# Kernel tuning notes

Measured on AMD Instinct MI355X. Metric: run time of the kernel, lower is better.

The kernel has to match this reference:

```python
import jax, jax.numpy as jnp
import numpy as np

N_HEAD = 16
N_EMBD = 2048
HEAD_DIM = N_EMBD // N_HEAD


def setup_inputs() -> dict:
    key = jax.random.key(0)
    kx, kqkv, kp = jax.random.split(key, 3)
    B, S = 2, 2048
    x = jax.random.normal(kx, (B, S, N_EMBD), dtype=jnp.float32)
    # torch nn.Linear weights, stored as [out, in]; y = x @ W.T
    scale = 1.0 / np.sqrt(N_EMBD)
    Wqkv = jax.random.uniform(kqkv, (3 * N_EMBD, N_EMBD), dtype=jnp.float32, minval=-scale, maxval=scale)
    Wproj = jax.random.uniform(kp, (N_EMBD, N_EMBD), dtype=jnp.float32, minval=-scale, maxval=scale)
    return {"x": x, "Wqkv": Wqkv, "Wproj": Wproj}


def reference(x, Wqkv, Wproj):
    B, S, E = x.shape
    qkv = x @ Wqkv.T  # [B,S,3E]
    q, k, v = jnp.split(qkv, 3, axis=2)
    # [B,H,S,D]
    q = q.reshape(B, S, N_HEAD, HEAD_DIM).transpose(0, 2, 1, 3)
    k = k.reshape(B, S, N_HEAD, HEAD_DIM).transpose(0, 2, 1, 3)
    v = v.reshape(B, S, N_HEAD, HEAD_DIM).transpose(0, 2, 1, 3)
    scores = jnp.einsum('bhqd,bhkd->bhqk', q, k) / jnp.sqrt(jnp.float32(HEAD_DIM))
    causal = jnp.tril(jnp.ones((S, S), dtype=bool))  # [S,S]
    scores = jnp.where(causal[None, None, :, :], scores, -jnp.inf)
    weights = jax.nn.softmax(scores, axis=-1)
    out = jnp.einsum('bhqk,bhkd->bhqd', weights, v)  # [B,H,S,D]
    out = out.transpose(0, 2, 1, 3).reshape(B, S, E)
    return out @ Wproj.T
```

## Files before the change

kernel.cpp:

```cpp
#include <hip/hip_runtime.h>
#include <cstdint>
#include <cstddef>

typedef __bf16 bf16;
typedef __bf16 bf16x8 __attribute__((ext_vector_type(8)));
typedef float  f32x4  __attribute__((ext_vector_type(4)));

static_assert(sizeof(bf16x8) == 16, "bf16x8 must be 16B");

__device__ __forceinline__ void async_copy16(const bf16* g, bf16* l) {
  __builtin_amdgcn_global_load_lds(
      (__attribute__((address_space(1))) void*)(g),
      (__attribute__((address_space(3))) void*)(l),
      16, 0, 0);
}

__global__ __launch_bounds__(256)
void conv_f32_bf16(const float* __restrict__ s, bf16* __restrict__ d) {
  const size_t i = ((size_t)blockIdx.x * 256 + threadIdx.x) * 8;
  const f32x4 a = *(const f32x4*)(s + i);
  const f32x4 b = *(const f32x4*)(s + i + 4);
  bf16x8 o;
#pragma unroll
  for (int e = 0; e < 4; ++e) { o[e] = (bf16)a[e]; o[4 + e] = (bf16)b[e]; }
  *(bf16x8*)(d + i) = o;
}

template<int AMODE>
__device__ __forceinline__ void stage_half(const bf16* __restrict__ P, int K,
                                           int row0, int k0, int ks,
                                           bf16* lds, int wave, int lane) {
#pragma unroll
  for (int i = 0; i < 2; ++i) {
    const int lin0 = i * 512 + wave * 64;
    const int lin  = lin0 + lane;
    const int row  = lin >> 2;
    const int ch   = lin & 3;
    const int gch  = ch ^ ((row >> 1) & 3);
    const bf16* src;
    if constexpr (AMODE == 2) {
      const int rowA = row0 + row;
      const int b = rowA >> 11, s = rowA & 2047;
      const int kk = k0 + ks * 32;
      src = P + ((size_t)(b * 16 + (kk >> 7)) * 2048 + s) * 128 + (kk & 127) + gch * 8;
    } else {
      src = P + (size_t)(row0 + row) * K + k0 + ks * 32 + gch * 8;
    }
    async_copy16(src, lds + ks * 8192 + lin0 * 8);
  }
}

template<int AMODE, int CMODE>
__global__ __launch_bounds__(512, 2)
void gemm256(const bf16* __restrict__ A, const bf16* __restrict__ W,
             float* __restrict__ Crow, bf16* __restrict__ Cq,
             bf16* __restrict__ Ck, bf16* __restrict__ Cvt,
             int M, int N, int K, int nbase) {
  __shared__ bf16 As[2 * 16384];
  __shared__ bf16 Ws[2 * 16384];

  const int tid  = threadIdx.x;
  const int wave = tid >> 6, lane = tid & 63;
  const int quad = lane >> 4, r = lane & 15;
  const int wr = wave >> 2, wc = wave & 3;

  const int gx  = gridDim.x;
  const int nwg = gx * gridDim.y;
  int wg = blockIdx.y * gx + blockIdx.x;
  wg = (wg & 7) * (nwg >> 3) + (wg >> 3);
  const int m0 = (wg / gx) * 256;
  const int n0 = (wg % gx) * 256;

  const int wm = wr * 128;
  const int wn = wc * 64;
  const int nT = K >> 6;

  f32x4 acc[8][4] = {};

  stage_half<AMODE>(A, K, m0, 0, 0, As, wave, lane);
  stage_half<0>   (W, K, n0, 0, 0, Ws, wave, lane);
  stage_half<AMODE>(A, K, m0, 0, 1, As, wave, lane);
  stage_half<0>   (W, K, n0, 0, 1, Ws, wave, lane);
  if (nT > 1) {
    stage_half<AMODE>(A, K, m0, 64, 0, As + 16384, wave, lane);
    stage_half<0>   (W, K, n0, 64, 0, Ws + 16384, wave, lane);
    asm volatile("s_waitcnt vmcnt(4)" ::: "memory");
  } else {
    asm volatile("s_waitcnt vmcnt(0)" ::: "memory");
  }
  __builtin_amdgcn_s_barrier();

  for (int t = 0; t < nT; ++t) {
    const int c = t & 1;
    bf16* Ab = As + c * 16384;
    bf16* Wb = Ws + c * 16384;
    bf16* An = As + (c ^ 1) * 16384;
    bf16* Wn = Ws + (c ^ 1) * 16384;
    bf16x8 af[4], bfr[4];
#pragma unroll
    for (int ph = 0; ph < 4; ++ph) {
      const int ks = ph >> 1, mh = ph & 1;
      if (mh == 0) {
#pragma unroll
        for (int n = 0; n < 4; ++n) {
          const int br = wn + n * 16 + r;
          bfr[n] = *(const bf16x8*)(Wb + ks * 8192 + br * 32 + ((quad ^ ((br >> 1) & 3)) << 3));
        }
      }
#pragma unroll
      for (int m = 0; m < 4; ++m) {
        const int ar = wm + mh * 64 + m * 16 + r;
        af[m] = *(const bf16x8*)(Ab + ks * 8192 + ar * 32 + ((quad ^ ((ar >> 1) & 3)) << 3));
      }
      if (ph == 0) {
        if (t + 1 < nT) stage_half<AMODE>(A, K, m0, (t + 1) << 6, 1, An, wave, lane);
      } else if (ph == 1) {
        if (t + 1 < nT) stage_half<0>(W, K, n0, (t + 1) << 6, 1, Wn, wave, lane);
      } else if (ph == 2) {
        if (t + 2 < nT) stage_half<AMODE>(A, K, m0, (t + 2) << 6, 0, Ab, wave, lane);
      } else {
        if (t + 2 < nT) {
          stage_half<0>(W, K, n0, (t + 2) << 6, 0, Wb, wave, lane);
          __builtin_amdgcn_sched_barrier(0);
          asm volatile("s_waitcnt vmcnt(4)" ::: "memory");
        } else if (t + 1 < nT) {
          __builtin_amdgcn_sched_barrier(0);
          asm volatile("s_waitcnt vmcnt(0)" ::: "memory");
        }
      }
      __builtin_amdgcn_s_barrier();
      asm volatile("s_waitcnt lgkmcnt(0)" ::: "memory");
      __builtin_amdgcn_sched_barrier(0);
      __builtin_amdgcn_s_setprio(1);
#pragma unroll
      for (int m = 0; m < 4; ++m)
#pragma unroll
        for (int n = 0; n < 4; ++n)
          acc[mh * 4 + m][n] =
              __builtin_amdgcn_mfma_f32_16x16x32_bf16(af[m], bfr[n], acc[mh * 4 + m][n], 0, 0, 0);
      __builtin_amdgcn_s_setprio(0);
      __builtin_amdgcn_s_barrier();
    }
  }

#pragma unroll
  for (int i = 0; i < 8; ++i) {
    const int growb = m0 + wm + i * 16 + quad * 4;
#pragma unroll
    for (int j = 0; j < 4; ++j) {
      const int gcol = n0 + wn + j * 16 + r;
#pragma unroll
      for (int rg = 0; rg < 4; ++rg) {
        const int grow = growb + rg;
        if constexpr (CMODE == 1) {
          const int gc = nbase + gcol;
          const int which = gc >> 11;
          const int h = (gc >> 7) & 15;
          const int d = gc & 127;
          const int b = grow >> 11;
          const int s = grow & 2047;
          const bf16 v = (bf16)acc[i][j][rg];
          if (which == 0)
            Cq[(((size_t)b * 16 + h) * 2048 + s) * 128 + d] = v;
          else if (which == 1)
            Ck[(((size_t)b * 16 + h) * 2048 + s) * 128 + d] = v;
          else
            Cvt[(((size_t)b * 16 + h) * 128 + d) * 2048 + s] = v;
        } else {
          Crow[(size_t)grow * N + gcol] = acc[i][j][rg];
        }
      }
    }
  }
}

__global__ __launch_bounds__(512, 2)
void attn_kernel(bf16* __restrict__ Q, const bf16* __restrict__ K,
                 const bf16* __restrict__ Vt, int S) {
  __shared__ bf16 k_lds[2][64 * 128];
  __shared__ bf16 v_lds[2][128 * 64];
  __shared__ bf16 p_lds[8][16 * 64];

  const int tid = threadIdx.x, wave = tid >> 6, lane = tid & 63;
  const int quad = lane >> 4, r = lane & 15;
  const int bh = blockIdx.y;
  bf16* Qh = Q + (size_t)bh * S * 128;
  const bf16* Kh = K + (size_t)bh * S * 128;
  const bf16* Vth = Vt + (size_t)bh * 128 * S;

  const float sc = 0.0883883476483184f * 1.4426950408889634f;

  auto issue_stage = [&](int kv0, int buf) {
#pragma unroll
    for (int j = 0; j < 2; ++j) {
      const int lin0 = j * 512 + wave * 64;
      const int lin = lin0 + lane;
      const int row = lin >> 4, ch = lin & 15;
      async_copy16(Kh + (size_t)(kv0 + row) * 128 + ((ch ^ (row & 7)) << 3),
                   &k_lds[buf][0] + lin0 * 8);
    }
#pragma unroll
    for (int j = 0; j < 2; ++j) {
      const int lin0 = j * 512 + wave * 64;
      const int lin = lin0 + lane;
      const int row = lin >> 3, c = lin & 7;
      async_copy16(Vth + (size_t)row * S + kv0 + ((c ^ (row & 7)) << 3),
                   &v_lds[buf][0] + lin0 * 8);
    }
  };

  for (int pass = 0; pass < 2; ++pass) {
    const int qb = pass ? blockIdx.x : (15 - blockIdx.x);
    const int q0 = qb << 7;
    const int qrow0 = q0 + wave * 16;
    const int nkv = (q0 + 128) >> 6;

    bf16x8 qf[4];
    for (int ks = 0; ks < 4; ++ks)
      qf[ks] = *(const bf16x8*)(Qh + (size_t)(qrow0 + r) * 128 + ks * 32 + quad * 8);

    f32x4 o_acc[8] = {};
    f32x4 m_run, l_run;
    for (int t = 0; t < 4; ++t) { m_run[t] = -1e30f; l_run[t] = 0.f; }

    issue_stage(0, 0);

    for (int kt = 0; kt < nkv; ++kt) {
      const int kv0 = kt << 6;
      const int cur = kt & 1;
      if (kt + 1 < nkv) {
        issue_stage((kt + 1) << 6, cur ^ 1);
        asm volatile("s_waitcnt vmcnt(4)" ::: "memory");
      } else {
        asm volatile("s_waitcnt vmcnt(0)" ::: "memory");
      }
      __builtin_amdgcn_sched_barrier(0);
      __syncthreads();

      if (kv0 <= qrow0 + 15) {
        f32x4 sa[4] = {};
        __builtin_amdgcn_s_setprio(1);
        for (int ks = 0; ks < 4; ++ks) {
          bf16x8 kf[4];
          for (int nt = 0; nt < 4; ++nt) {
            const int kr = nt * 16 + r;
            kf[nt] = *(const bf16x8*)(&k_lds[cur][0] + kr * 128 + (((ks * 4 + quad) ^ (kr & 7)) << 3));
          }
          for (int nt = 0; nt < 4; ++nt)
            sa[nt] = __builtin_amdgcn_mfma_f32_16x16x32_bf16(qf[ks], kf[nt], sa[nt], 0, 0, 0);
        }
        __builtin_amdgcn_s_setprio(0);
        if (kv0 + 63 > qrow0) {
          for (int nt = 0; nt < 4; ++nt) {
            const int col  = kv0 + nt * 16 + r;
            const int rowb = qrow0 + quad * 4;
            for (int rg = 0; rg < 4; ++rg)
              if (col > rowb + rg) sa[nt][rg] = -1e30f;
          }
        }
        f32x4 mx = sa[0];
        for (int nt = 1; nt < 4; ++nt)
          for (int rg = 0; rg < 4; ++rg) mx[rg] = fmaxf(mx[rg], sa[nt][rg]);
        for (int off = 1; off < 16; off <<= 1)
          for (int rg = 0; rg < 4; ++rg) mx[rg] = fmaxf(mx[rg], __shfl_xor(mx[rg], off, 64));
        float need = mx[0] - m_run[0];
        for (int rg = 1; rg < 4; ++rg) need = fmaxf(need, mx[rg] - m_run[rg]);
        if (need * sc > 8.0f) {
          f32x4 alpha;
          for (int rg = 0; rg < 4; ++rg) {
            const float mnew = fmaxf(m_run[rg], mx[rg]);
            alpha[rg] = exp2f((m_run[rg] - mnew) * sc);
            m_run[rg] = mnew;
            l_run[rg] *= alpha[rg];
          }
          for (int nt2 = 0; nt2 < 8; ++nt2)
            for (int rg = 0; rg < 4; ++rg) o_acc[nt2][rg] *= alpha[rg];
        }
        f32x4 rsum = {0.f, 0.f, 0.f, 0.f};
        for (int nt = 0; nt < 4; ++nt)
          for (int rg = 0; rg < 4; ++rg) {
            const float p = exp2f((sa[nt][rg] - m_run[rg]) * sc);
            sa[nt][rg] = p;
            rsum[rg] += p;
          }
        for (int off = 1; off < 16; off <<= 1)
          for (int rg = 0; rg < 4; ++rg) rsum[rg] += __shfl_xor(rsum[rg], off, 64);
        for (int rg = 0; rg < 4; ++rg) l_run[rg] += rsum[rg];
        for (int nt = 0; nt < 4; ++nt)
          for (int rg = 0; rg < 4; ++rg) {
            const int prow = quad * 4 + rg;
            const int pcol = nt * 16 + r;
            p_lds[wave][prow * 64 + (((pcol >> 3) ^ (prow & 7)) * 8) + (pcol & 7)] =
                (bf16)sa[nt][rg];
          }
        __builtin_amdgcn_s_setprio(1);
        for (int ks2 = 0; ks2 < 2; ++ks2) {
          const int prow = r;
          const bf16x8 pf = *(const bf16x8*)(p_lds[wave] + prow * 64 + (((ks2 * 4 + quad) ^ (prow & 7)) * 8));
          for (int nt2 = 0; nt2 < 8; ++nt2) {
            const int vrow = nt2 * 16 + r;
            const bf16x8 vf = *(const bf16x8*)(&v_lds[cur][0] + vrow * 64 + (((ks2 * 4 + quad) ^ (vrow & 7)) * 8));
            o_acc[nt2] = __builtin_amdgcn_mfma_f32_16x16x32_bf16(pf, vf, o_acc[nt2], 0, 0, 0);
          }
        }
        __builtin_amdgcn_s_setprio(0);
      }
      __syncthreads();
    }

    f32x4 inv;
    for (int rg = 0; rg < 4; ++rg) inv[rg] = 1.0f / l_run[rg];
    for (int nt2 = 0; nt2 < 8; ++nt2) {
      const int d = nt2 * 16 + r;
      for (int rg = 0; rg < 4; ++rg) {
        const int s = qrow0 + quad * 4 + rg;
        Qh[(size_t)s * 128 + d] = (bf16)(o_acc[nt2][rg] * inv[rg]);
      }
    }
  }
}

extern "C" void kernel_launch(void* const* d_in, const int* in_sizes, int n_in,
                              void* d_out, int out_size, void* d_ws, size_t ws_size,
                              hipStream_t stream) {
  const float* x     = (const float*)d_in[0];
  const float* Wqkv  = (const float*)d_in[1];
  const float* Wproj = (const float*)d_in[2];
  float* out = (float*)d_out;

  const int Bm = 4096, E = 2048;
  const size_t plane = 8388608;

  bf16* qw  = (bf16*)d_ws;
  bf16* vtw = qw + plane;
  bf16* xb  = vtw + plane;
  bf16* kw  = (bf16*)d_out;
  bf16* wqb = kw + plane;

  conv_f32_bf16<<<8388608 / 2048, 256, 0, stream>>>(x, xb);
  conv_f32_bf16<<<6291456 / 2048, 256, 0, stream>>>(Wqkv, wqb);
  gemm256<0, 1><<<dim3(3072 / 256, Bm / 256), 512, 0, stream>>>(
      xb, wqb, nullptr, qw, kw, vtw, Bm, 3072, E, 0);
  conv_f32_bf16<<<6291456 / 2048, 256, 0, stream>>>(Wqkv + 6291456, wqb);
  gemm256<0, 1><<<dim3(3072 / 256, Bm / 256), 512, 0, stream>>>(
      xb, wqb, nullptr, qw, kw, vtw, Bm, 3072, E, 3072);
  attn_kernel<<<dim3(8, 32), 512, 0, stream>>>(qw, kw, vtw, 2048);
  conv_f32_bf16<<<4194304 / 2048, 256, 0, stream>>>(Wproj, xb);
  gemm256<2, 0><<<dim3(2048 / 256, Bm / 256), 512, 0, stream>>>(
      qw, xb, out, nullptr, nullptr, nullptr, Bm, 2048, E, 0);
}
```

Measured before the change: 450.2 us.

## Switch projection GEMMs to 128x256 tiles with two-phase inline-asm LDS pipeline

Replaces the 256x256 GEMM with a 128x256 tile: each wave now owns 64x64 of output and reads its fragments through inline ds_read_b128 with immediate offsets. The K loop runs in two phases, each staging the next A and W halves together. The QKV projection is now split into three 2048-column chunks instead of two 3072-column chunks, giving more workgroups per launch (256 vs 192 for the QKV chunks, 256 vs 128 for the output projection) to fill the CUs. In exchange, each tile reuses less data, so global traffic per FLOP rises, and there are more kernel launches.

```diff
diff --git a/kernel.cpp b/kernel.cpp
--- a/kernel.cpp
+++ b/kernel.cpp
@@ -13,6 +13,10 @@
       (__attribute__((address_space(1))) void*)(g),
       (__attribute__((address_space(3))) void*)(l),
       16, 0, 0);
+}
+
+__device__ __forceinline__ uint32_t lds_u32(const bf16* p) {
+  return (uint32_t)(uintptr_t)((__attribute__((address_space(3))) const bf16*)p);
 }
 
 __global__ __launch_bounds__(256)
@@ -27,9 +31,29 @@
 }
 
 template<int AMODE>
-__device__ __forceinline__ void stage_half(const bf16* __restrict__ P, int K,
-                                           int row0, int k0, int ks,
-                                           bf16* lds, int wave, int lane) {
+__device__ __forceinline__ void stageA(const bf16* __restrict__ P, int K,
+                                       int row0, int k0, int ks,
+                                       bf16* lds, int wave, int lane) {
+  const int lin0 = wave * 64;
+  const int lin  = lin0 + lane;
+  const int row  = lin >> 2;
+  const int ch   = lin & 3;
+  const int gch  = ch ^ ((row >> 1) & 3);
+  const bf16* src;
+  if constexpr (AMODE == 2) {
+    const int rowA = row0 + row;
+    const int b = rowA >> 11, s = rowA & 2047;
+    const int kk = k0 + ks * 32;
+    src = P + ((size_t)(b * 16 + (kk >> 7)) * 2048 + s) * 128 + (kk & 127) + gch * 8;
+  } else {
+    src = P + (size_t)(row0 + row) * K + k0 + ks * 32 + gch * 8;
+  }
+  async_copy16(src, lds + ks * 4096 + lin0 * 8);
+}
+
+__device__ __forceinline__ void stageW(const bf16* __restrict__ P, int K,
+                                       int row0, int k0, int ks,
+                                       bf16* lds, int wave, int lane) {
 #pragma unroll
   for (int i = 0; i < 2; ++i) {
     const int lin0 = i * 512 + wave * 64;
@@ -37,27 +61,31 @@
     const int row  = lin >> 2;
     const int ch   = lin & 3;
     const int gch  = ch ^ ((row >> 1) & 3);
-    const bf16* src;
-    if constexpr (AMODE == 2) {
-      const int rowA = row0 + row;
-      const int b = rowA >> 11, s = rowA & 2047;
-      const int kk = k0 + ks * 32;
-      src = P + ((size_t)(b * 16 + (kk >> 7)) * 2048 + s) * 128 + (kk & 127) + gch * 8;
-    } else {
-      src = P + (size_t)(row0 + row) * K + k0 + ks * 32 + gch * 8;
-    }
-    async_copy16(src, lds + ks * 8192 + lin0 * 8);
-  }
+    async_copy16(P + (size_t)(row0 + row) * K + k0 + ks * 32 + gch * 8,
+                 lds + ks * 8192 + lin0 * 8);
+  }
+}
+
+__device__ __forceinline__ void ld_frags(uint32_t ab, uint32_t bb,
+                                         bf16x8 (&a)[4], bf16x8 (&b)[4]) {
+  asm volatile("ds_read_b128 %0, %1 offset:0"    : "=v"(a[0]) : "v"(ab));
+  asm volatile("ds_read_b128 %0, %1 offset:1024" : "=v"(a[1]) : "v"(ab));
+  asm volatile("ds_read_b128 %0, %1 offset:2048" : "=v"(a[2]) : "v"(ab));
+  asm volatile("ds_read_b128 %0, %1 offset:3072" : "=v"(a[3]) : "v"(ab));
+  asm volatile("ds_read_b128 %0, %1 offset:0"    : "=v"(b[0]) : "v"(bb));
+  asm volatile("ds_read_b128 %0, %1 offset:1024" : "=v"(b[1]) : "v"(bb));
+  asm volatile("ds_read_b128 %0, %1 offset:2048" : "=v"(b[2]) : "v"(bb));
+  asm volatile("ds_read_b128 %0, %1 offset:3072" : "=v"(b[3]) : "v"(bb));
 }
 
 template<int AMODE, int CMODE>
 __global__ __launch_bounds__(512, 2)
-void gemm256(const bf16* __restrict__ A, const bf16* __restrict__ W,
-             float* __restrict__ Crow, bf16* __restrict__ Cq,
-             bf16* __restrict__ Ck, bf16* __restrict__ Cvt,
-             int M, int N, int K, int nbase) {
-  __shared__ bf16 As[2 * 16384];
-  __shared__ bf16 Ws[2 * 16384];
+void gemm_bt2(const bf16* __restrict__ A, const bf16* __restrict__ W,
+              float* __restrict__ Crow, bf16* __restrict__ Cq,
+              bf16* __restrict__ Ck, bf16* __restrict__ Cvt,
+              int M, int N, int K, int nbase) {
+  __shared__ bf16 As[2][2][128 * 32];
+  __shared__ bf16 Ws[2][2][256 * 32];
 
   const int tid  = threadIdx.x;
   const int wave = tid >> 6, lane = tid & 63;
@@ -68,83 +96,82 @@
   const int nwg = gx * gridDim.y;
   int wg = blockIdx.y * gx + blockIdx.x;
   wg = (wg & 7) * (nwg >> 3) + (wg >> 3);
-  const int m0 = (wg / gx) * 256;
+  const int m0 = (wg / gx) * 128;
   const int n0 = (wg % gx) * 256;
 
-  const int wm = wr * 128;
-  const int wn = wc * 64;
+  const int wm = wr * 64, wn = wc * 64;
   const int nT = K >> 6;
-
-  f32x4 acc[8][4] = {};
-
-  stage_half<AMODE>(A, K, m0, 0, 0, As, wave, lane);
-  stage_half<0>   (W, K, n0, 0, 0, Ws, wave, lane);
-  stage_half<AMODE>(A, K, m0, 0, 1, As, wave, lane);
-  stage_half<0>   (W, K, n0, 0, 1, Ws, wave, lane);
+  const int cs = quad ^ ((r >> 1) & 3);
+
+  f32x4 acc[4][4] = {};
+
+  const uint32_t a_rd = lds_u32(&As[0][0][0]) + (((wm + r) * 32 + cs * 8) << 1);
+  const uint32_t b_rd = lds_u32(&Ws[0][0][0]) + (((wn + r) * 32 + cs * 8) << 1);
+
+  stageA<AMODE>(A, K, m0, 0, 0, &As[0][0][0], wave, lane);
+  stageW(W, K, n0, 0, 0, &Ws[0][0][0], wave, lane);
+  stageA<AMODE>(A, K, m0, 0, 1, &As[0][0][0], wave, lane);
+  stageW(W, K, n0, 0, 1, &Ws[0][0][0], wave, lane);
   if (nT > 1) {
-    stage_half<AMODE>(A, K, m0, 64, 0, As + 16384, wave, lane);
-    stage_half<0>   (W, K, n0, 64, 0, Ws + 16384, wave, lane);
-    asm volatile("s_waitcnt vmcnt(4)" ::: "memory");
+    stageA<AMODE>(A, K, m0, 64, 0, &As[1][0][0], wave, lane);
+    stageW(W, K, n0, 64, 0, &Ws[1][0][0], wave, lane);
+    asm volatile("s_waitcnt vmcnt(6)" ::: "memory");
   } else {
-    asm volatile("s_waitcnt vmcnt(0)" ::: "memory");
+    asm volatile("s_waitcnt vmcnt(3)" ::: "memory");
   }
   __builtin_amdgcn_s_barrier();
 
   for (int t = 0; t < nT; ++t) {
     const int c = t & 1;
-    bf16* Ab = As + c * 16384;
-    bf16* Wb = Ws + c * 16384;
-    bf16* An = As + (c ^ 1) * 16384;
-    bf16* Wn = Ws + (c ^ 1) * 16384;
-    bf16x8 af[4], bfr[4];
-#pragma unroll
-    for (int ph = 0; ph < 4; ++ph) {
-      const int ks = ph >> 1, mh = ph & 1;
-      if (mh == 0) {
-#pragma unroll
-        for (int n = 0; n < 4; ++n) {
-          const int br = wn + n * 16 + r;
-          bfr[n] = *(const bf16x8*)(Wb + ks * 8192 + br * 32 + ((quad ^ ((br >> 1) & 3)) << 3));
-        }
-      }
-#pragma unroll
-      for (int m = 0; m < 4; ++m) {
-        const int ar = wm + mh * 64 + m * 16 + r;
-        af[m] = *(const bf16x8*)(Ab + ks * 8192 + ar * 32 + ((quad ^ ((ar >> 1) & 3)) << 3));
-      }
-      if (ph == 0) {
-        if (t + 1 < nT) stage_half<AMODE>(A, K, m0, (t + 1) << 6, 1, An, wave, lane);
-      } else if (ph == 1) {
-        if (t + 1 < nT) stage_half<0>(W, K, n0, (t + 1) << 6, 1, Wn, wave, lane);
-      } else if (ph == 2) {
-        if (t + 2 < nT) stage_half<AMODE>(A, K, m0, (t + 2) << 6, 0, Ab, wave, lane);
-      } else {
-        if (t + 2 < nT) {
-          stage_half<0>(W, K, n0, (t + 2) << 6, 0, Wb, wave, lane);
-          __builtin_amdgcn_sched_barrier(0);
-          asm volatile("s_waitcnt vmcnt(4)" ::: "memory");
-        } else if (t + 1 < nT) {
-          __builtin_amdgcn_sched_barrier(0);
-          asm volatile("s_waitcnt vmcnt(0)" ::: "memory");
-        }
-      }
-      __builtin_amdgcn_s_barrier();
-      asm volatile("s_waitcnt lgkmcnt(0)" ::: "memory");
-      __builtin_amdgcn_sched_barrier(0);
-      __builtin_amdgcn_s_setprio(1);
-#pragma unroll
-      for (int m = 0; m < 4; ++m)
-#pragma unroll
-        for (int n = 0; n < 4; ++n)
-          acc[mh * 4 + m][n] =
-              __builtin_amdgcn_mfma_f32_16x16x32_bf16(af[m], bfr[n], acc[mh * 4 + m][n], 0, 0, 0);
-      __builtin_amdgcn_s_setprio(0);
-      __builtin_amdgcn_s_barrier();
-    }
-  }
-
-#pragma unroll
-  for (int i = 0; i < 8; ++i) {
+    bf16x8 af[4], bw[4];
+
+    ld_frags(a_rd + (c * 2 + 0) * 8192, b_rd + (c * 2 + 0) * 16384, af, bw);
+    if (t + 1 < nT) {
+      stageA<AMODE>(A, K, m0, (t + 1) << 6, 1, &As[c ^ 1][0][0], wave, lane);
+      stageW(W, K, n0, (t + 1) << 6, 1, &Ws[c ^ 1][0][0], wave, lane);
+      asm volatile("s_waitcnt vmcnt(6)" ::: "memory");
+    } else {
+      asm volatile("s_waitcnt vmcnt(0)" ::: "memory");
+    }
+    __builtin_amdgcn_sched_barrier(0);
+    __builtin_amdgcn_s_barrier();
+    asm volatile("s_waitcnt lgkmcnt(0)" ::: "memory");
+    __builtin_amdgcn_sched_barrier(0);
+    __builtin_amdgcn_s_setprio(1);
+#pragma unroll
+    for (int m = 0; m < 4; ++m)
+#pragma unroll
+      for (int n = 0; n < 4; ++n)
+        acc[m][n] = __builtin_amdgcn_mfma_f32_16x16x32_bf16(af[m], bw[n], acc[m][n], 0, 0, 0);
+    __builtin_amdgcn_s_setprio(0);
+    __builtin_amdgcn_s_barrier();
+
+    ld_frags(a_rd + (c * 2 + 1) * 8192, b_rd + (c * 2 + 1) * 16384, af, bw);
+    if (t + 2 < nT) {
+      stageA<AMODE>(A, K, m0, (t + 2) << 6, 0, &As[c][0][0], wave, lane);
+      stageW(W, K, n0, (t + 2) << 6, 0, &Ws[c][0][0], wave, lane);
+      asm volatile("s_waitcnt vmcnt(6)" ::: "memory");
+    } else if (t + 1 < nT) {
+      asm volatile("s_waitcnt vmcnt(3)" ::: "memory");
+    } else {
+      asm volatile("s_waitcnt vmcnt(0)" ::: "memory");
+    }
+    __builtin_amdgcn_sched_barrier(0);
+    __builtin_amdgcn_s_barrier();
+    asm volatile("s_waitcnt lgkmcnt(0)" ::: "memory");
+    __builtin_amdgcn_sched_barrier(0);
+    __builtin_amdgcn_s_setprio(1);
+#pragma unroll
+    for (int m = 0; m < 4; ++m)
+#pragma unroll
+      for (int n = 0; n < 4; ++n)
+        acc[m][n] = __builtin_amdgcn_mfma_f32_16x16x32_bf16(af[m], bw[n], acc[m][n], 0, 0, 0);
+    __builtin_amdgcn_s_setprio(0);
+    __builtin_amdgcn_s_barrier();
+  }
+
+#pragma unroll
+  for (int i = 0; i < 4; ++i) {
     const int growb = m0 + wm + i * 16 + quad * 4;
 #pragma unroll
     for (int j = 0; j < 4; ++j) {
@@ -338,14 +365,13 @@
   bf16* wqb = kw + plane;
 
   conv_f32_bf16<<<8388608 / 2048, 256, 0, stream>>>(x, xb);
-  conv_f32_bf16<<<6291456 / 2048, 256, 0, stream>>>(Wqkv, wqb);
-  gemm256<0, 1><<<dim3(3072 / 256, Bm / 256), 512, 0, stream>>>(
-      xb, wqb, nullptr, qw, kw, vtw, Bm, 3072, E, 0);
-  conv_f32_bf16<<<6291456 / 2048, 256, 0, stream>>>(Wqkv + 6291456, wqb);
-  gemm256<0, 1><<<dim3(3072 / 256, Bm / 256), 512, 0, stream>>>(
-      xb, wqb, nullptr, qw, kw, vtw, Bm, 3072, E, 3072);
+  for (int chunk = 0; chunk < 3; ++chunk) {
+    conv_f32_bf16<<<4194304 / 2048, 256, 0, stream>>>(Wqkv + (size_t)chunk * 4194304, wqb);
+    gemm_bt2<0, 1><<<dim3(2048 / 256, Bm / 128), 512, 0, stream>>>(
+        xb, wqb, nullptr, qw, kw, vtw, Bm, 2048, E, chunk * 2048);
+  }
   attn_kernel<<<dim3(8, 32), 512, 0, stream>>>(qw, kw, vtw, 2048);
   conv_f32_bf16<<<4194304 / 2048, 256, 0, stream>>>(Wproj, xb);
-  gemm256<2, 0><<<dim3(2048 / 256, Bm / 256), 512, 0, stream>>>(
+  gemm_bt2<2, 0><<<dim3(2048 / 256, Bm / 128), 512, 0, stream>>>(
       qw, xb, out, nullptr, nullptr, nullptr, Bm, 2048, E, 0);
 }
```

Result: faster. 413.5 us (-8.1%).
